# Kernel tuning notes

Hardware: AMD Instinct MI355X
Metric: run time of the kernel (lower is better)

The kernel has to match this reference:

```python
import jax, jax.numpy as jnp
import numpy as np

N_NODE = 100000
DEPTH = 10
N_EDGE = 1600000
D_FEAT = 32
BASE_ALPHA = 1.0


def setup_inputs() -> dict:
    key = jax.random.key(0)
    k1, k2 = jax.random.split(key)
    x = jax.random.normal(k1, (N_NODE, D_FEAT), dtype=jnp.float32)
    edge_index = jax.random.randint(k2, (2, N_EDGE), 0, N_NODE, dtype=jnp.int64)
    edge_attr = jnp.ones((N_EDGE,), dtype=jnp.float32)
    # alphas init: min(1/alpha, 1) = 1.0 for each of depth+1 coefficients
    alphas = jnp.ones((DEPTH + 1,), dtype=jnp.float32)
    return {"x": x, "edge_index": edge_index, "edge_attr": edge_attr, "alphas": alphas}


def reference(x, edge_index, edge_attr, alphas):
    n_node = x.shape[0]
    row, col = edge_index[0], edge_index[1]

    # GCN normalization: val = deg^-1/2[row] * w * deg^-1/2[col]
    deg = jax.ops.segment_sum(jnp.ones_like(edge_attr), row, num_segments=n_node)
    deg = jnp.where(deg < 0.5, deg + 1.0, deg)
    dinv = deg ** -0.5
    val = dinv[row] * edge_attr * dinv[col]  # (E,)

    def adj_mul(h):  # sparse A @ h via gather + segment_sum (coalesce-equivalent)
        return jax.ops.segment_sum(val[:, None] * h[col], row, num_segments=n_node)

    alphas_t = BASE_ALPHA * jnp.tanh(alphas)  # (depth+1,)

    # PowerConv (monomial basis): x_0 = x; x_L = alpha_L * (A @ x_{L-1})
    xs = [x]
    for L in range(1, DEPTH + 1):
        xs.append(alphas_t[L] * adj_mul(xs[-1]))
    return jnp.stack(xs, axis=1)  # (n_node, depth+1, d_feat)
```

## Files before the change

### kernel.cpp

```cpp
#include <hip/hip_runtime.h>
#include <math.h>

#define N_NODE 100000
#define DEPTH  10
#define N_EDGE 1600000
#define D_FEAT 32
#define D_OUT  ((DEPTH + 1) * D_FEAT)
#define NB_SCAN ((N_NODE + 255) / 256)

__global__ void count_kernel(const int* __restrict__ row, int* __restrict__ cnt, int E) {
    int e = blockIdx.x * blockDim.x + threadIdx.x;
    if (e < E) atomicAdd(&cnt[row[e]], 1);
}

__device__ inline int wave_incl_scan(int v) {
    int lane = threadIdx.x & 63;
    #pragma unroll
    for (int off = 1; off < 64; off <<= 1) {
        int t = __shfl_up(v, off, 64);
        if (lane >= off) v += t;
    }
    return v;
}

__global__ void blockscan_kernel(const int* __restrict__ cnt, int* __restrict__ rowStart,
                                 int* __restrict__ blockSums, int n) {
    __shared__ int partials[4];
    int i = blockIdx.x * 256 + threadIdx.x;
    int v = (i < n) ? cnt[i] : 0;
    int incl = wave_incl_scan(v);
    int wid = threadIdx.x >> 6, lane = threadIdx.x & 63;
    if (lane == 63) partials[wid] = incl;
    __syncthreads();
    int woff = 0;
    #pragma unroll
    for (int w = 0; w < 4; ++w) woff += (w < wid) ? partials[w] : 0;
    if (i < n) rowStart[i] = woff + incl - v;
    if (threadIdx.x == 255) blockSums[blockIdx.x] = woff + incl;
}

__global__ void scansums_kernel(int* __restrict__ blockSums, int nb) {
    __shared__ int partials[8];
    int i = threadIdx.x;
    int v = (i < nb) ? blockSums[i] : 0;
    int incl = wave_incl_scan(v);
    int wid = i >> 6, lane = i & 63;
    if (lane == 63) partials[wid] = incl;
    __syncthreads();
    int woff = 0;
    #pragma unroll
    for (int w = 0; w < 8; ++w) woff += (w < wid) ? partials[w] : 0;
    if (i < nb) blockSums[i] = woff + incl - v;
    if (i == 511) blockSums[nb] = woff + incl;
}

__global__ void addoffs_kernel(int* __restrict__ rowStart, const int* __restrict__ blockSums,
                               int n, int nb) {
    int i = blockIdx.x * 256 + threadIdx.x;
    if (i < n)  rowStart[i] += blockSums[i >> 8];
    if (i == n) rowStart[n] = blockSums[nb];
}

__global__ void dinv_kernel(const int* __restrict__ cnt, float* __restrict__ dinv, int n) {
    int i = blockIdx.x * blockDim.x + threadIdx.x;
    if (i < n) {
        float d = (float)cnt[i];
        if (d < 0.5f) d += 1.0f;
        dinv[i] = 1.0f / sqrtf(d);
    }
}

__global__ void scatter_kernel(const int* __restrict__ row, const int* __restrict__ col,
                               const float* __restrict__ eattr,
                               const int* __restrict__ rowStart, int* __restrict__ cnt,
                               const float* __restrict__ dinv,
                               int2* __restrict__ csr, int E) {
    int e = blockIdx.x * blockDim.x + threadIdx.x;
    if (e < E) {
        int r = row[e], c = col[e];
        int p = rowStart[r] + atomicSub(&cnt[r], 1) - 1;
        float val = dinv[r] * eattr[e] * dinv[c];
        csr[p] = make_int2(c, __float_as_int(val));
    }
}

__global__ void alpha_kernel(const float* __restrict__ alphas, float* __restrict__ alphaT) {
    int i = threadIdx.x;
    if (i <= DEPTH) alphaT[i] = tanhf(alphas[i]);
}

__global__ void copyx_kernel(const float4* __restrict__ x4, float4* __restrict__ out4) {
    int i = blockIdx.x * blockDim.x + threadIdx.x;
    if (i < N_NODE * 8) {
        int node = i >> 3, q = i & 7;
        out4[(size_t)node * 88 + q] = x4[i];
    }
}

__global__ __launch_bounds__(256) void spmm_kernel(const int* __restrict__ rowStart,
                                                   const int2* __restrict__ csr,
                                                   const float* __restrict__ alphaT,
                                                   int L, float* __restrict__ out) {
    int rowid = (int)((blockIdx.x * 256 + threadIdx.x) >> 6);
    if (rowid >= N_NODE) return;
    int lane = threadIdx.x & 63;
    int s = lane >> 3;
    int q = lane & 7;

    int start = rowStart[rowid];
    int end   = rowStart[rowid + 1];

    const float4* __restrict__ out4 = (const float4*)out;
    int prev = (L - 1) * 8 + q;

    float4 acc = make_float4(0.f, 0.f, 0.f, 0.f);
    for (int e = start + s; e < end; e += 8) {
        int2  cv = csr[e];
        float v  = __int_as_float(cv.y);
        float4 h = out4[(size_t)cv.x * 88 + prev];
        acc.x += v * h.x; acc.y += v * h.y; acc.z += v * h.z; acc.w += v * h.w;
    }

    #pragma unroll
    for (int m = 8; m < 64; m <<= 1) {
        acc.x += __shfl_xor(acc.x, m, 64);
        acc.y += __shfl_xor(acc.y, m, 64);
        acc.z += __shfl_xor(acc.z, m, 64);
        acc.w += __shfl_xor(acc.w, m, 64);
    }

    if (s == 0) {
        float a = alphaT[L];
        float4 r = make_float4(a * acc.x, a * acc.y, a * acc.z, a * acc.w);
        ((float4*)out)[(size_t)rowid * 88 + L * 8 + q] = r;
    }
}

extern "C" void kernel_launch(void* const* d_in, const int* in_sizes, int n_in,
                              void* d_out, int out_size, void* d_ws, size_t ws_size,
                              hipStream_t stream) {
    const float* x      = (const float*)d_in[0];
    const int*   eidx   = (const int*)d_in[1];
    const float* eattr  = (const float*)d_in[2];
    const float* alphas = (const float*)d_in[3];
    float* out = (float*)d_out;

    const int* row = eidx;
    const int* col = eidx + N_EDGE;

    char* p = (char*)d_ws;
    auto alloc = [&](size_t bytes) { char* r = p; p += (bytes + 255) & ~(size_t)255; return (void*)r; };
    int*   cnt       = (int*)  alloc((size_t)N_NODE * 4);
    int*   rowStart  = (int*)  alloc((size_t)(N_NODE + 1) * 4);
    int*   blockSums = (int*)  alloc((size_t)(NB_SCAN + 1) * 4);
    float* dinv      = (float*)alloc((size_t)N_NODE * 4);
    float* alphaT    = (float*)alloc(64);
    int2*  csr       = (int2*) alloc((size_t)N_EDGE * 8);
    (void)ws_size; (void)in_sizes; (void)n_in; (void)out_size;

    hipMemsetAsync(cnt, 0, (size_t)N_NODE * 4, stream);

    const int TB = 256;
    int eBlocks = (N_EDGE + TB - 1) / TB;
    int nBlocks = (N_NODE + TB - 1) / TB;

    count_kernel<<<eBlocks, TB, 0, stream>>>(row, cnt, N_EDGE);
    blockscan_kernel<<<NB_SCAN, TB, 0, stream>>>(cnt, rowStart, blockSums, N_NODE);
    scansums_kernel<<<1, 512, 0, stream>>>(blockSums, NB_SCAN);
    addoffs_kernel<<<(N_NODE + 1 + TB - 1) / TB, TB, 0, stream>>>(rowStart, blockSums, N_NODE, NB_SCAN);
    dinv_kernel<<<nBlocks, TB, 0, stream>>>(cnt, dinv, N_NODE);
    scatter_kernel<<<eBlocks, TB, 0, stream>>>(row, col, eattr, rowStart, cnt, dinv, csr, N_EDGE);
    alpha_kernel<<<1, 64, 0, stream>>>(alphas, alphaT);
    copyx_kernel<<<(N_NODE * 8 + TB - 1) / TB, TB, 0, stream>>>((const float4*)x, (float4*)out);

    int spmmBlocks = (N_NODE * 64 + TB - 1) / TB;
    for (int L = 1; L <= DEPTH; ++L) {
        spmm_kernel<<<spmmBlocks, TB, 0, stream>>>(rowStart, csr, alphaT, L, out);
    }
}
```

Baseline: 543.2 us.

## Gather SpMM inputs from compact bf16 ping-pong feature buffers

Each layer's output is also written as a compact bf16 copy in a dense node-major buffer (64 B per node), and the next layer gathers neighbor features from it instead of from the strided fp32 output tensor. This shrinks the random-gather working set so it is far more likely to stay in cache, and halves the bytes per gather. The risk is bf16 rounding error compounding across ten propagation steps, plus extra writes for the bf16 copy.

```diff
diff --git a/kernel.cpp b/kernel.cpp
--- a/kernel.cpp
+++ b/kernel.cpp
@@ -7,6 +7,15 @@
 #define D_FEAT 32
 #define D_OUT  ((DEPTH + 1) * D_FEAT)
 #define NB_SCAN ((N_NODE + 255) / 256)
+
+__device__ inline unsigned short f32_to_bf16(float f) {
+    unsigned int b = __float_as_uint(f);
+    unsigned int r = (b + 0x7FFFu + ((b >> 16) & 1u)) >> 16;
+    return (unsigned short)r;
+}
+__device__ inline float bf16_to_f32(unsigned short u) {
+    return __uint_as_float(((unsigned int)u) << 16);
+}
 
 __global__ void count_kernel(const int* __restrict__ row, int* __restrict__ cnt, int E) {
     int e = blockIdx.x * blockDim.x + threadIdx.x;
@@ -89,18 +98,25 @@
     if (i <= DEPTH) alphaT[i] = tanhf(alphas[i]);
 }
 
-__global__ void copyx_kernel(const float4* __restrict__ x4, float4* __restrict__ out4) {
+__global__ void copyx_kernel(const float4* __restrict__ x4, float4* __restrict__ out4,
+                             ushort4* __restrict__ h0) {
     int i = blockIdx.x * blockDim.x + threadIdx.x;
     if (i < N_NODE * 8) {
         int node = i >> 3, q = i & 7;
-        out4[(size_t)node * 88 + q] = x4[i];
+        float4 v = x4[i];
+        out4[(size_t)node * 88 + q] = v;
+        h0[i] = make_ushort4(f32_to_bf16(v.x), f32_to_bf16(v.y),
+                             f32_to_bf16(v.z), f32_to_bf16(v.w));
     }
 }
 
 __global__ __launch_bounds__(256) void spmm_kernel(const int* __restrict__ rowStart,
                                                    const int2* __restrict__ csr,
                                                    const float* __restrict__ alphaT,
-                                                   int L, float* __restrict__ out) {
+                                                   int L,
+                                                   const ushort4* __restrict__ h_prev,
+                                                   ushort4* __restrict__ h_cur,
+                                                   float* __restrict__ out) {
     int rowid = (int)((blockIdx.x * 256 + threadIdx.x) >> 6);
     if (rowid >= N_NODE) return;
     int lane = threadIdx.x & 63;
@@ -110,15 +126,15 @@
     int start = rowStart[rowid];
     int end   = rowStart[rowid + 1];
 
-    const float4* __restrict__ out4 = (const float4*)out;
-    int prev = (L - 1) * 8 + q;
-
     float4 acc = make_float4(0.f, 0.f, 0.f, 0.f);
     for (int e = start + s; e < end; e += 8) {
-        int2  cv = csr[e];
-        float v  = __int_as_float(cv.y);
-        float4 h = out4[(size_t)cv.x * 88 + prev];
-        acc.x += v * h.x; acc.y += v * h.y; acc.z += v * h.z; acc.w += v * h.w;
+        int2    cv = csr[e];
+        float   v  = __int_as_float(cv.y);
+        ushort4 h  = h_prev[(size_t)cv.x * 8 + q];
+        acc.x += v * bf16_to_f32(h.x);
+        acc.y += v * bf16_to_f32(h.y);
+        acc.z += v * bf16_to_f32(h.z);
+        acc.w += v * bf16_to_f32(h.w);
     }
 
     #pragma unroll
@@ -133,6 +149,11 @@
         float a = alphaT[L];
         float4 r = make_float4(a * acc.x, a * acc.y, a * acc.z, a * acc.w);
         ((float4*)out)[(size_t)rowid * 88 + L * 8 + q] = r;
+        if (L < DEPTH) {
+            h_cur[(size_t)rowid * 8 + q] =
+                make_ushort4(f32_to_bf16(r.x), f32_to_bf16(r.y),
+                             f32_to_bf16(r.z), f32_to_bf16(r.w));
+        }
     }
 }
 
@@ -150,12 +171,14 @@
 
     char* p = (char*)d_ws;
     auto alloc = [&](size_t bytes) { char* r = p; p += (bytes + 255) & ~(size_t)255; return (void*)r; };
-    int*   cnt       = (int*)  alloc((size_t)N_NODE * 4);
-    int*   rowStart  = (int*)  alloc((size_t)(N_NODE + 1) * 4);
-    int*   blockSums = (int*)  alloc((size_t)(NB_SCAN + 1) * 4);
-    float* dinv      = (float*)alloc((size_t)N_NODE * 4);
-    float* alphaT    = (float*)alloc(64);
-    int2*  csr       = (int2*) alloc((size_t)N_EDGE * 8);
+    int*     cnt       = (int*)    alloc((size_t)N_NODE * 4);
+    int*     rowStart  = (int*)    alloc((size_t)(N_NODE + 1) * 4);
+    int*     blockSums = (int*)    alloc((size_t)(NB_SCAN + 1) * 4);
+    float*   dinv      = (float*)  alloc((size_t)N_NODE * 4);
+    float*   alphaT    = (float*)  alloc(64);
+    ushort4* h0        = (ushort4*)alloc((size_t)N_NODE * 64);
+    ushort4* h1        = (ushort4*)alloc((size_t)N_NODE * 64);
+    int2*    csr       = (int2*)   alloc((size_t)N_EDGE * 8);
     (void)ws_size; (void)in_sizes; (void)n_in; (void)out_size;
 
     hipMemsetAsync(cnt, 0, (size_t)N_NODE * 4, stream);
@@ -171,10 +194,12 @@
     dinv_kernel<<<nBlocks, TB, 0, stream>>>(cnt, dinv, N_NODE);
     scatter_kernel<<<eBlocks, TB, 0, stream>>>(row, col, eattr, rowStart, cnt, dinv, csr, N_EDGE);
     alpha_kernel<<<1, 64, 0, stream>>>(alphas, alphaT);
-    copyx_kernel<<<(N_NODE * 8 + TB - 1) / TB, TB, 0, stream>>>((const float4*)x, (float4*)out);
+    copyx_kernel<<<(N_NODE * 8 + TB - 1) / TB, TB, 0, stream>>>((const float4*)x, (float4*)out, h0);
 
     int spmmBlocks = (N_NODE * 64 + TB - 1) / TB;
     for (int L = 1; L <= DEPTH; ++L) {
-        spmm_kernel<<<spmmBlocks, TB, 0, stream>>>(rowStart, csr, alphaT, L, out);
-    }
-}
+        const ushort4* hp = (L & 1) ? h0 : h1;
+        ushort4*       hc = (L & 1) ? h1 : h0;
+        spmm_kernel<<<spmmBlocks, TB, 0, stream>>>(rowStart, csr, alphaT, L, hp, hc, out);
+    }
+}
```

Result: no change. 549.9 us (+1.2%).

## Propagate intermediate SpMM features in packed bf16 buffers with nontemporal stores

Applied to the files above, without the earlier changes.

Each layer now reads the previous layer's features from a compact bf16 ping-pong buffer (64 bytes per node) instead of the strided fp32 output, which halves the gather bytes and improves locality. Each lane handles 8 features, so 16 edges are processed in parallel per row. Output and CSR writes use nontemporal stores. In exchange it adds an extra bf16 write per layer and bf16 rounding error that compounds across the 10 layers.

```diff
diff --git a/kernel.cpp b/kernel.cpp
--- a/kernel.cpp
+++ b/kernel.cpp
@@ -7,6 +7,19 @@
 #define D_FEAT 32
 #define D_OUT  ((DEPTH + 1) * D_FEAT)
 #define NB_SCAN ((N_NODE + 255) / 256)
+
+typedef float        f32x4 __attribute__((ext_vector_type(4)));
+typedef unsigned int u32x4 __attribute__((ext_vector_type(4)));
+typedef int          i32x2 __attribute__((ext_vector_type(2)));
+
+__device__ inline unsigned short f32_to_bf16(float f) {
+    unsigned int b = __float_as_uint(f);
+    unsigned int r = (b + 0x7FFFu + ((b >> 16) & 1u)) >> 16;
+    return (unsigned short)r;
+}
+__device__ inline unsigned int pack_bf16x2(float lo, float hi) {
+    return (unsigned int)f32_to_bf16(lo) | ((unsigned int)f32_to_bf16(hi) << 16);
+}
 
 __global__ void count_kernel(const int* __restrict__ row, int* __restrict__ cnt, int E) {
     int e = blockIdx.x * blockDim.x + threadIdx.x;
@@ -74,13 +87,14 @@
                                const float* __restrict__ eattr,
                                const int* __restrict__ rowStart, int* __restrict__ cnt,
                                const float* __restrict__ dinv,
-                               int2* __restrict__ csr, int E) {
+                               i32x2* __restrict__ csr, int E) {
     int e = blockIdx.x * blockDim.x + threadIdx.x;
     if (e < E) {
         int r = row[e], c = col[e];
         int p = rowStart[r] + atomicSub(&cnt[r], 1) - 1;
         float val = dinv[r] * eattr[e] * dinv[c];
-        csr[p] = make_int2(c, __float_as_int(val));
+        i32x2 ent; ent.x = c; ent.y = __float_as_int(val);
+        __builtin_nontemporal_store(ent, &csr[p]);
     }
 }
 
@@ -89,50 +103,72 @@
     if (i <= DEPTH) alphaT[i] = tanhf(alphas[i]);
 }
 
-__global__ void copyx_kernel(const float4* __restrict__ x4, float4* __restrict__ out4) {
+__global__ void copyx_kernel(const f32x4* __restrict__ x4, f32x4* __restrict__ out4,
+                             unsigned int* __restrict__ h0) {
     int i = blockIdx.x * blockDim.x + threadIdx.x;
     if (i < N_NODE * 8) {
         int node = i >> 3, q = i & 7;
-        out4[(size_t)node * 88 + q] = x4[i];
+        f32x4 v = x4[i];
+        __builtin_nontemporal_store(v, &out4[(size_t)node * 88 + q]);
+        h0[i * 2]     = pack_bf16x2(v.x, v.y);
+        h0[i * 2 + 1] = pack_bf16x2(v.z, v.w);
     }
 }
 
 __global__ __launch_bounds__(256) void spmm_kernel(const int* __restrict__ rowStart,
-                                                   const int2* __restrict__ csr,
+                                                   const i32x2* __restrict__ csr,
                                                    const float* __restrict__ alphaT,
-                                                   int L, float* __restrict__ out) {
+                                                   int L,
+                                                   const u32x4* __restrict__ h_prev,
+                                                   u32x4* __restrict__ h_cur,
+                                                   f32x4* __restrict__ out4) {
     int rowid = (int)((blockIdx.x * 256 + threadIdx.x) >> 6);
     if (rowid >= N_NODE) return;
     int lane = threadIdx.x & 63;
-    int s = lane >> 3;
-    int q = lane & 7;
+    int s = lane >> 2;
+    int q = lane & 3;
 
     int start = rowStart[rowid];
     int end   = rowStart[rowid + 1];
 
-    const float4* __restrict__ out4 = (const float4*)out;
-    int prev = (L - 1) * 8 + q;
-
-    float4 acc = make_float4(0.f, 0.f, 0.f, 0.f);
-    for (int e = start + s; e < end; e += 8) {
-        int2  cv = csr[e];
+    float acc[8] = {0.f, 0.f, 0.f, 0.f, 0.f, 0.f, 0.f, 0.f};
+    for (int e = start + s; e < end; e += 16) {
+        i32x2 cv = __builtin_nontemporal_load(&csr[e]);
         float v  = __int_as_float(cv.y);
-        float4 h = out4[(size_t)cv.x * 88 + prev];
-        acc.x += v * h.x; acc.y += v * h.y; acc.z += v * h.z; acc.w += v * h.w;
-    }
-
-    #pragma unroll
-    for (int m = 8; m < 64; m <<= 1) {
-        acc.x += __shfl_xor(acc.x, m, 64);
-        acc.y += __shfl_xor(acc.y, m, 64);
-        acc.z += __shfl_xor(acc.z, m, 64);
-        acc.w += __shfl_xor(acc.w, m, 64);
+        u32x4 h  = h_prev[(size_t)cv.x * 4 + q];
+        acc[0] += v * __uint_as_float(h.x << 16);
+        acc[1] += v * __uint_as_float(h.x & 0xFFFF0000u);
+        acc[2] += v * __uint_as_float(h.y << 16);
+        acc[3] += v * __uint_as_float(h.y & 0xFFFF0000u);
+        acc[4] += v * __uint_as_float(h.z << 16);
+        acc[5] += v * __uint_as_float(h.z & 0xFFFF0000u);
+        acc[6] += v * __uint_as_float(h.w << 16);
+        acc[7] += v * __uint_as_float(h.w & 0xFFFF0000u);
+    }
+
+    #pragma unroll
+    for (int m = 4; m < 64; m <<= 1) {
+        #pragma unroll
+        for (int k = 0; k < 8; ++k) acc[k] += __shfl_xor(acc[k], m, 64);
     }
 
     if (s == 0) {
         float a = alphaT[L];
-        float4 r = make_float4(a * acc.x, a * acc.y, a * acc.z, a * acc.w);
-        ((float4*)out)[(size_t)rowid * 88 + L * 8 + q] = r;
+        #pragma unroll
+        for (int k = 0; k < 8; ++k) acc[k] *= a;
+        size_t ob = (size_t)rowid * 88 + L * 8 + q * 2;
+        f32x4 o0; o0.x = acc[0]; o0.y = acc[1]; o0.z = acc[2]; o0.w = acc[3];
+        f32x4 o1; o1.x = acc[4]; o1.y = acc[5]; o1.z = acc[6]; o1.w = acc[7];
+        __builtin_nontemporal_store(o0, &out4[ob]);
+        __builtin_nontemporal_store(o1, &out4[ob + 1]);
+        if (L < DEPTH) {
+            u32x4 hh;
+            hh.x = pack_bf16x2(acc[0], acc[1]);
+            hh.y = pack_bf16x2(acc[2], acc[3]);
+            hh.z = pack_bf16x2(acc[4], acc[5]);
+            hh.w = pack_bf16x2(acc[6], acc[7]);
+            __builtin_nontemporal_store(hh, &h_cur[(size_t)rowid * 4 + q]);
+        }
     }
 }
 
@@ -155,10 +191,12 @@
     int*   blockSums = (int*)  alloc((size_t)(NB_SCAN + 1) * 4);
     float* dinv      = (float*)alloc((size_t)N_NODE * 4);
     float* alphaT    = (float*)alloc(64);
-    int2*  csr       = (int2*) alloc((size_t)N_EDGE * 8);
+    u32x4* h0        = (u32x4*)alloc((size_t)N_NODE * 64);
+    u32x4* h1        = (u32x4*)alloc((size_t)N_NODE * 64);
+    i32x2* csr       = (i32x2*)alloc((size_t)N_EDGE * 8);
     (void)ws_size; (void)in_sizes; (void)n_in; (void)out_size;
 
-    hipMemsetAsync(cnt, 0, (size_t)N_NODE * 4, stream);
+    (void)hipMemsetAsync(cnt, 0, (size_t)N_NODE * 4, stream);
 
     const int TB = 256;
     int eBlocks = (N_EDGE + TB - 1) / TB;
@@ -171,10 +209,14 @@
     dinv_kernel<<<nBlocks, TB, 0, stream>>>(cnt, dinv, N_NODE);
     scatter_kernel<<<eBlocks, TB, 0, stream>>>(row, col, eattr, rowStart, cnt, dinv, csr, N_EDGE);
     alpha_kernel<<<1, 64, 0, stream>>>(alphas, alphaT);
-    copyx_kernel<<<(N_NODE * 8 + TB - 1) / TB, TB, 0, stream>>>((const float4*)x, (float4*)out);
+    copyx_kernel<<<(N_NODE * 8 + TB - 1) / TB, TB, 0, stream>>>((const f32x4*)x, (f32x4*)out,
+                                                                (unsigned int*)h0);
 
     int spmmBlocks = (N_NODE * 64 + TB - 1) / TB;
     for (int L = 1; L <= DEPTH; ++L) {
-        spmm_kernel<<<spmmBlocks, TB, 0, stream>>>(rowStart, csr, alphaT, L, out);
-    }
-}
+        const u32x4* hp = (L & 1) ? h0 : h1;
+        u32x4*       hc = (L & 1) ? h1 : h0;
+        spmm_kernel<<<spmmBlocks, TB, 0, stream>>>(rowStart, csr, alphaT, L, hp, hc,
+                                                   (f32x4*)out);
+    }
+}
```

Result: slower. 593.6 us (+9.3%).
